# Kernel tuning notes

Hardware: AMD Instinct MI355X
Metric: run time of the kernel (lower is better)

## Reference

```python
import jax, jax.numpy as jnp
import numpy as np

MAX_SEQ = 512
HIDDEN = 1024
E = 2 * HIDDEN  # expansion
S = 128         # head dim s
EPS = 1e-5


def setup_inputs() -> dict:
    key = jax.random.key(0)
    ks = jax.random.split(key, 10)
    B, N = 32, 512
    x = jax.random.normal(ks[0], (B, N, HIDDEN), dtype=jnp.float32)
    attention_mask = jnp.ones((B, N), dtype=jnp.float32)
    gamma = jax.random.uniform(ks[1], (2, S), dtype=jnp.float32)
    beta = jax.random.uniform(ks[2], (2, S), dtype=jnp.float32)
    w = jax.random.uniform(ks[3], (2 * MAX_SEQ - 1,), dtype=jnp.float32)
    a_p = jax.random.uniform(ks[4], (1, S), dtype=jnp.float32)
    b_p = jax.random.uniform(ks[5], (1, S), dtype=jnp.float32)
    # uv: Linear(hidden -> 2e+s), stored input-major for x @ uv_w
    uv_w = jax.random.normal(ks[6], (HIDDEN, 2 * E + S), dtype=jnp.float32) * 0.02
    uv_b = jnp.zeros((2 * E + S,), dtype=jnp.float32)
    o_w = jax.random.normal(ks[7], (E, HIDDEN), dtype=jnp.float32) * 0.02
    o_b = jnp.zeros((HIDDEN,), dtype=jnp.float32)
    ln_g = jnp.ones((HIDDEN,), dtype=jnp.float32)
    ln_b = jnp.zeros((HIDDEN,), dtype=jnp.float32)
    return {"x": x, "attention_mask": attention_mask, "gamma": gamma, "beta": beta,
            "w": w, "a_p": a_p, "b_p": b_p, "uv_w": uv_w, "uv_b": uv_b,
            "o_w": o_w, "o_b": o_b, "ln_g": ln_g, "ln_b": ln_b}


def _rope_seq(x):
    # x: [b, n, 2, s]; rotary positions along axis 1 (matches module's rope(x, dim=1))
    n, d = x.shape[1], x.shape[-1]
    half = d // 2
    pos = jnp.arange(n, dtype=jnp.float32)
    # inv_freq = 10000 ** (arange(half)/half)  (freq_seq = -arange/half, inv = 10000**-freq_seq)
    inv_freq = jnp.power(10000.0, jnp.arange(half, dtype=jnp.float32) / half)
    sinusoid = pos[:, None] * inv_freq  # [n, half]
    sin = jnp.sin(sinusoid)[None, :, None, :]
    cos = jnp.cos(sinusoid)[None, :, None, :]
    x1, x2 = jnp.split(x, 2, axis=-1)
    return jnp.concatenate([x1 * cos - x2 * sin, x2 * cos + x1 * sin], axis=-1)


def _rel_pos_bias(w, seq_len):
    # Toeplitz trick (max_seq_length <= 512 path)
    t = jnp.pad(w[: 2 * MAX_SEQ - 1], (0, MAX_SEQ))          # [3S-1]
    t = jnp.tile(t, MAX_SEQ)[: -MAX_SEQ].reshape(-1, MAX_SEQ, 3 * MAX_SEQ - 2)
    r = (2 * MAX_SEQ - 1) // 2
    t = t[..., r:-r]                                          # [1, S, S]
    return t[:, :seq_len, :seq_len]


def reference(x, attention_mask, gamma, beta, w, a_p, b_p, uv_w, uv_b, o_w, o_b, ln_g, ln_b):
    n = x.shape[1]
    shortcut = x
    mu = jnp.mean(x, axis=-1, keepdims=True)
    var = jnp.mean(jnp.square(x - mu), axis=-1, keepdims=True)
    xn = (x - mu) * jax.lax.rsqrt(var + EPS) * ln_g + ln_b
    uv = jax.nn.silu(xn @ uv_w + uv_b)                        # [b, n, 2e+s]
    u, v, base = jnp.split(uv, [E, 2 * E], axis=-1)
    base = base[..., None, :] * gamma + beta                  # [b, n, 2, s]
    base = _rope_seq(base)
    q, k = base[:, :, 0], base[:, :, 1]                       # [b, n, s]
    qk = jnp.einsum('bnd,bmd->bnm', q, k)
    qk = qk + ((1.0 - attention_mask) * -1e12)[:, None, :]
    bias = _rel_pos_bias(w, n)                                # [1, n, n]
    kernel = jnp.square(jax.nn.relu(qk / MAX_SEQ + bias))
    out = u * jnp.einsum('bnm,bme->bne', kernel, v)           # [b, n, e]
    return out @ o_w + o_b + shortcut
```

## Files before the change

### kernel.cpp

```cpp
#include <hip/hip_runtime.h>
#include <math.h>

#define HIDDEN 1024
#define NSEQ   512
#define BATCH  32
#define EDIM   2048
#define SDIM   128
#define UVN    (2 * EDIM + SDIM)

using short8  = __attribute__((ext_vector_type(8))) short;
using float4x = __attribute__((ext_vector_type(4))) float;

__device__ __forceinline__ ushort f2bf(float f) {
    unsigned u = __float_as_uint(f);
    u += 0x7FFFu + ((u >> 16) & 1u);
    return (ushort)(u >> 16);
}
__device__ __forceinline__ float bf2f(ushort h) {
    return __uint_as_float(((unsigned)h) << 16);
}

#define ASYNC16(gp, lp) __builtin_amdgcn_global_load_lds( \
    (const __attribute__((address_space(1))) unsigned int*)(unsigned long long)(const void*)(gp), \
    (__attribute__((address_space(3))) unsigned int*)(unsigned int)(unsigned long long)(const void*)(lp), \
    16, 0, 0)

__global__ __launch_bounds__(64) void tab_kernel(float* __restrict__ sin_t,
                                                 float* __restrict__ cos_t) {
    int i = blockIdx.x;
    int j = threadIdx.x;
    double inv = pow(10000.0, (double)j / 64.0);
    double ang = (double)i * inv;
    sin_t[i * 64 + j] = (float)sin(ang);
    cos_t[i * 64 + j] = (float)cos(ang);
}

__global__ __launch_bounds__(256) void transpose_f32_bf16(const float* __restrict__ src,
                                                          ushort* __restrict__ dst,
                                                          int R, int Cc) {
    __shared__ float tile[32][33];
    const int bx = blockIdx.x;
    const int by = blockIdx.y;
    const int lx = threadIdx.x & 31;
    const int gy = threadIdx.x >> 5;
#pragma unroll
    for (int i = 0; i < 4; ++i) {
        int r = by * 32 + gy + i * 8;
        tile[gy + i * 8][lx] = src[(size_t)r * Cc + bx * 32 + lx];
    }
    __syncthreads();
#pragma unroll
    for (int i = 0; i < 4; ++i) {
        int c = bx * 32 + gy + i * 8;
        dst[(size_t)c * R + by * 32 + lx] = f2bf(tile[lx][gy + i * 8]);
    }
}

__global__ __launch_bounds__(256) void ln_kernel(const float* __restrict__ x,
                                                 const float* __restrict__ g,
                                                 const float* __restrict__ b,
                                                 ushort* __restrict__ xn) {
    const size_t t = blockIdx.x;
    const int tid = threadIdx.x;
    const float4 v = ((const float4*)(x + t * HIDDEN))[tid];
    float s = v.x + v.y + v.z + v.w;
#pragma unroll
    for (int off = 32; off > 0; off >>= 1) s += __shfl_down(s, off);
    __shared__ float red[4];
    const int wid = tid >> 6, lane = tid & 63;
    if (lane == 0) red[wid] = s;
    __syncthreads();
    const float mean = (red[0] + red[1] + red[2] + red[3]) * (1.0f / HIDDEN);
    __syncthreads();
    const float dx = v.x - mean, dy = v.y - mean, dz = v.z - mean, dw = v.w - mean;
    float s2 = dx * dx + dy * dy + dz * dz + dw * dw;
#pragma unroll
    for (int off = 32; off > 0; off >>= 1) s2 += __shfl_down(s2, off);
    if (lane == 0) red[wid] = s2;
    __syncthreads();
    const float var = (red[0] + red[1] + red[2] + red[3]) * (1.0f / HIDDEN);
    const float rs = rsqrtf(var + 1e-5f);
    const float4 gv = ((const float4*)g)[tid];
    const float4 bv = ((const float4*)b)[tid];
    ushort4 o;
    o.x = f2bf(dx * rs * gv.x + bv.x);
    o.y = f2bf(dy * rs * gv.y + bv.y);
    o.z = f2bf(dz * rs * gv.z + bv.z);
    o.w = f2bf(dw * rs * gv.w + bv.w);
    ((ushort4*)(xn + t * HIDDEN))[tid] = o;
}

__device__ __forceinline__ void mfma_core_128(const ushort* __restrict__ A,
                                              const ushort* __restrict__ Bt,
                                              const int lda, const int ldb, const int K,
                                              const int m0, const int n0,
                                              ushort* As, ushort* Bs,
                                              float4x (&acc)[4][4]) {
    const int tid = threadIdx.x;
    const int l = tid & 63, w = tid >> 6;
    const int wm = (w & 1) << 6, wn = (w >> 1) << 6;

    const int c0 = w * 128 + l;
    const int r0 = c0 >> 2, kc0 = (c0 & 3) * 8;
    const int c1 = c0 + 64;
    const int r1 = c1 >> 2, kc1 = (c1 & 3) * 8;
    char* ldsA0 = (char*)As + (size_t)(w * 128) * 16;
    char* ldsA1 = ldsA0 + 1024;
    char* ldsB0 = (char*)Bs + (size_t)(w * 128) * 16;
    char* ldsB1 = ldsB0 + 1024;
    const ushort* gA0 = A + (size_t)(m0 + r0) * lda + kc0;
    const ushort* gA1 = A + (size_t)(m0 + r1) * lda + kc1;
    const ushort* gB0 = Bt + (size_t)(n0 + r0) * ldb + kc0;
    const ushort* gB1 = Bt + (size_t)(n0 + r1) * ldb + kc1;

    const int lr = l & 15, lk = (l >> 4) * 8;
    int aoff[4], boff[4];
#pragma unroll
    for (int i = 0; i < 4; ++i) {
        aoff[i] = (wm + i * 16 + lr) * 32 + lk;
        boff[i] = (wn + i * 16 + lr) * 32 + lk;
    }

    for (int k0 = 0; k0 < K; k0 += 32) {
        __syncthreads();
        ASYNC16(gA0 + k0, ldsA0);
        ASYNC16(gA1 + k0, ldsA1);
        ASYNC16(gB0 + k0, ldsB0);
        ASYNC16(gB1 + k0, ldsB1);
        __syncthreads();
        short8 af[4], bfr[4];
#pragma unroll
        for (int i = 0; i < 4; ++i) af[i] = *(const short8*)(As + aoff[i]);
#pragma unroll
        for (int i = 0; i < 4; ++i) bfr[i] = *(const short8*)(Bs + boff[i]);
#pragma unroll
        for (int mi = 0; mi < 4; ++mi)
#pragma unroll
            for (int ni = 0; ni < 4; ++ni)
                acc[mi][ni] = __builtin_amdgcn_mfma_f32_16x16x32_bf16(
                    af[mi], bfr[ni], acc[mi][ni], 0, 0, 0);
    }
}

template <typename F>
__device__ __forceinline__ void epilogue_loop(const float4x (&acc)[4][4],
                                              int m0, int n0, F body) {
    const int l = threadIdx.x & 63, w = threadIdx.x >> 6;
    const int wm = (w & 1) << 6, wn = (w >> 1) << 6;
    const int lrow = (l >> 4) << 2, lcol = l & 15;
#pragma unroll
    for (int mi = 0; mi < 4; ++mi)
#pragma unroll
        for (int ni = 0; ni < 4; ++ni)
#pragma unroll
            for (int r = 0; r < 4; ++r) {
                const int m = m0 + wm + mi * 16 + lrow + r;
                const int n = n0 + wn + ni * 16 + lcol;
                body(m, n, acc[mi][ni][r]);
            }
}

__device__ __forceinline__ void mfma_core_256(const ushort* __restrict__ A,
                                              const ushort* __restrict__ Bt,
                                              const int lda, const int ldb, const int K,
                                              const int m0, const int n0,
                                              char* smem,
                                              float4x (&acc)[8][4]) {
    const int tid = threadIdx.x;
    const int l = tid & 63, w = tid >> 6;
    const int wm = w >> 2, wn = w & 3;

    const int srow = l >> 2;
    const int kcol = (w & 1) * 32 + (((tid & 3) ^ ((l >> 3) & 3)) << 3);
    const int rb0  = w >> 1;
    const ushort* gA[4];
    const ushort* gB[4];
#pragma unroll
    for (int j = 0; j < 4; ++j) {
        const int row = (j * 4 + rb0) * 16 + srow;
        gA[j] = A  + (size_t)(m0 + row) * lda + kcol;
        gB[j] = Bt + (size_t)(n0 + row) * ldb + kcol;
    }
    char* const ldsA = smem;
    char* const ldsB = smem + 65536;
    const int wdst = w * 1024;

#define STG_A(buf, j, t)  ASYNC16(gA[j] + (size_t)(t) * 64, ldsA + (buf) * 32768 + (j) * 8192 + wdst)
#define STG_B(buf, j, t)  ASYNC16(gB[j] + (size_t)(t) * 64, ldsB + (buf) * 32768 + (j) * 8192 + wdst)
#define RAWBAR() do { __builtin_amdgcn_sched_barrier(0); __builtin_amdgcn_s_barrier(); \
                      __builtin_amdgcn_sched_barrier(0); } while (0)
#define WAITV(N) asm volatile("s_waitcnt vmcnt(" #N ")" ::: "memory")

    const int LB = (l & 15) * 64 + (((l >> 4) ^ ((l >> 1) & 3)) << 4);
    const int rbbA0 = wm * 4;
    const int rbbA1 = 8 + wm * 4;
    const int cbbB0 = wn * 2;
    const int cbbB1 = 8 + wn * 2;

    const int KT = K >> 6;

    STG_A(0, 0, 0); STG_A(0, 1, 0);
    STG_B(0, 0, 0); STG_B(0, 1, 0);
    STG_B(0, 2, 0); STG_B(0, 3, 0);
    STG_A(0, 2, 0); STG_A(0, 3, 0);
    STG_A(1, 0, 1); STG_A(1, 1, 1);
    STG_B(1, 0, 1); STG_B(1, 1, 1);
    STG_B(1, 2, 1); STG_B(1, 3, 1);
    WAITV(10);
    RAWBAR();

    for (int t = 0; t < KT; ++t) {
        const int buf = t & 1;
        const char* Ab = ldsA + buf * 32768;
        const char* Bb = ldsB + buf * 32768;
        short8 a[4][2], b0[2][2], b1[2][2];

#pragma unroll
        for (int mi = 0; mi < 4; ++mi) {
            a[mi][0] = *(const short8*)(Ab + (rbbA0 + mi) * 2048 + LB);
            a[mi][1] = *(const short8*)(Ab + (rbbA0 + mi) * 2048 + 1024 + LB);
        }
#pragma unroll
        for (int ni = 0; ni < 2; ++ni) {
            b0[ni][0] = *(const short8*)(Bb + (cbbB0 + ni) * 2048 + LB);
            b0[ni][1] = *(const short8*)(Bb + (cbbB0 + ni) * 2048 + 1024 + LB);
        }
        if (t + 1 < KT) { STG_A(buf ^ 1, 2, t + 1); STG_A(buf ^ 1, 3, t + 1); }
        RAWBAR();
        __builtin_amdgcn_s_setprio(1);
#pragma unroll
        for (int mi = 0; mi < 4; ++mi)
#pragma unroll
            for (int ni = 0; ni < 2; ++ni) {
                acc[mi][ni] = __builtin_amdgcn_mfma_f32_16x16x32_bf16(a[mi][0], b0[ni][0], acc[mi][ni], 0, 0, 0);
                acc[mi][ni] = __builtin_amdgcn_mfma_f32_16x16x32_bf16(a[mi][1], b0[ni][1], acc[mi][ni], 0, 0, 0);
            }
        __builtin_amdgcn_s_setprio(0);
        if (t < KT - 1) { WAITV(10); } else { WAITV(2); }
        RAWBAR();

#pragma unroll
        for (int ni = 0; ni < 2; ++ni) {
            b1[ni][0] = *(const short8*)(Bb + (cbbB1 + ni) * 2048 + LB);
            b1[ni][1] = *(const short8*)(Bb + (cbbB1 + ni) * 2048 + 1024 + LB);
        }
        if (t + 2 < KT) { STG_A(buf, 0, t + 2); STG_A(buf, 1, t + 2); }
        RAWBAR();
        __builtin_amdgcn_s_setprio(1);
#pragma unroll
        for (int mi = 0; mi < 4; ++mi)
#pragma unroll
            for (int ni = 0; ni < 2; ++ni) {
                acc[mi][2 + ni] = __builtin_amdgcn_mfma_f32_16x16x32_bf16(a[mi][0], b1[ni][0], acc[mi][2 + ni], 0, 0, 0);
                acc[mi][2 + ni] = __builtin_amdgcn_mfma_f32_16x16x32_bf16(a[mi][1], b1[ni][1], acc[mi][2 + ni], 0, 0, 0);
            }
        __builtin_amdgcn_s_setprio(0);
        if (t < KT - 2) { WAITV(10); } else if (t == KT - 2) { WAITV(8); } else { WAITV(0); }
        RAWBAR();

#pragma unroll
        for (int mi = 0; mi < 4; ++mi) {
            a[mi][0] = *(const short8*)(Ab + (rbbA1 + mi) * 2048 + LB);
            a[mi][1] = *(const short8*)(Ab + (rbbA1 + mi) * 2048 + 1024 + LB);
        }
        if (t + 2 < KT) {
            STG_B(buf, 0, t + 2); STG_B(buf, 1, t + 2);
            STG_B(buf, 2, t + 2); STG_B(buf, 3, t + 2);
        }
        RAWBAR();
        __builtin_amdgcn_s_setprio(1);
#pragma unroll
        for (int mi = 0; mi < 4; ++mi)
#pragma unroll
            for (int ni = 0; ni < 2; ++ni) {
                acc[4 + mi][2 + ni] = __builtin_amdgcn_mfma_f32_16x16x32_bf16(a[mi][0], b1[ni][0], acc[4 + mi][2 + ni], 0, 0, 0);
                acc[4 + mi][2 + ni] = __builtin_amdgcn_mfma_f32_16x16x32_bf16(a[mi][1], b1[ni][1], acc[4 + mi][2 + ni], 0, 0, 0);
            }
#pragma unroll
        for (int mi = 0; mi < 4; ++mi)
#pragma unroll
            for (int ni = 0; ni < 2; ++ni) {
                acc[4 + mi][ni] = __builtin_amdgcn_mfma_f32_16x16x32_bf16(a[mi][0], b0[ni][0], acc[4 + mi][ni], 0, 0, 0);
                acc[4 + mi][ni] = __builtin_amdgcn_mfma_f32_16x16x32_bf16(a[mi][1], b0[ni][1], acc[4 + mi][ni], 0, 0, 0);
            }
        __builtin_amdgcn_s_setprio(0);
        if (t < KT - 2) { WAITV(10); } else if (t == KT - 2) { WAITV(4); }
        RAWBAR();
    }
#undef STG_A
#undef STG_B
#undef RAWBAR
#undef WAITV
}

template <typename F>
__device__ __forceinline__ void epilogue_256(const float4x (&acc)[8][4],
                                             int m0, int n0, F body) {
    const int tid = threadIdx.x;
    const int l = tid & 63, w = tid >> 6;
    const int wm = w >> 2, wn = w & 3;
    const int lrow = (l >> 4) << 2, lcol = l & 15;
#pragma unroll
    for (int i = 0; i < 8; ++i)
#pragma unroll
        for (int j = 0; j < 4; ++j)
#pragma unroll
            for (int r = 0; r < 4; ++r) {
                const int m = m0 + (i >> 2) * 128 + wm * 64 + (i & 3) * 16 + lrow + r;
                const int n = n0 + (j >> 1) * 128 + wn * 32 + (j & 1) * 16 + lcol;
                body(m, n, acc[i][j][r]);
            }
}

__device__ __forceinline__ void mfma_core_v3(const ushort* __restrict__ A,
                                             const ushort* __restrict__ Bt,
                                             const int lda, const int ldb, const int K,
                                             const int m0, const int n0,
                                             char* smem,
                                             float4x (&acc)[4][4]) {
    const int tid = threadIdx.x;
    const int l = tid & 63, w = tid >> 6;
    const int wm = w >> 2, wn = w & 3;

    const int srow = l >> 2;
    const int kswz = ((l & 3) ^ ((l >> 3) & 3)) << 3;
    const ushort* gA = A + (size_t)(m0 + w * 16 + srow) * lda + kswz;
    const ushort* gB = Bt + (size_t)(n0 + w * 16 + srow) * ldb + kswz;
    char* const ldsA = smem;
    char* const ldsB = smem + 65536;
    const int woff = w * 2048;

    const int LB = (l & 15) * 64 + (((l >> 4) ^ ((l >> 1) & 3)) << 4);
    const int rbb = wm * 4, cbb = wn * 4;
    const int KT = K >> 6;

    ASYNC16(gA, ldsA + woff);
    ASYNC16(gA + 32, ldsA + woff + 1024);
    ASYNC16(gB, ldsB + woff);
    ASYNC16(gB + 32, ldsB + woff + 1024);
    __syncthreads();

    for (int t = 0; t < KT; ++t) {
        const int buf = t & 1;
        const char* Ab = ldsA + buf * 32768;
        const char* Bb = ldsB + buf * 32768;
        if (t + 1 < KT) {
            const size_t g = (size_t)(t + 1) * 64;
            char* dA = ldsA + (buf ^ 1) * 32768 + woff;
            char* dB = ldsB + (buf ^ 1) * 32768 + woff;
            ASYNC16(gA + g, dA);
            ASYNC16(gA + g + 32, dA + 1024);
            ASYNC16(gB + g, dB);
            ASYNC16(gB + g + 32, dB + 1024);
        }
        __builtin_amdgcn_sched_barrier(0);
#pragma unroll
        for (int kh = 0; kh < 2; ++kh) {
            short8 a[4], b[4];
#pragma unroll
            for (int i = 0; i < 4; ++i) {
                a[i] = *(const short8*)(Ab + (rbb + i) * 2048 + kh * 1024 + LB);
                b[i] = *(const short8*)(Bb + (cbb + i) * 2048 + kh * 1024 + LB);
            }
            __builtin_amdgcn_s_setprio(1);
#pragma unroll
            for (int i = 0; i < 4; ++i)
#pragma unroll
                for (int j = 0; j < 4; ++j)
                    acc[i][j] = __builtin_amdgcn_mfma_f32_16x16x32_bf16(
                        a[i], b[j], acc[i][j], 0, 0, 0);
            __builtin_amdgcn_s_setprio(0);
        }
        __syncthreads();
    }
}

template <typename F>
__device__ __forceinline__ void epilogue_v3(const float4x (&acc)[4][4],
                                            int m0, int n0, F body) {
    const int tid = threadIdx.x;
    const int l = tid & 63, w = tid >> 6;
    const int wm = w >> 2, wn = w & 3;
    const int lrow = (l >> 4) << 2, lcol = l & 15;
#pragma unroll
    for (int i = 0; i < 4; ++i)
#pragma unroll
        for (int j = 0; j < 4; ++j)
#pragma unroll
            for (int r = 0; r < 4; ++r) {
                const int m = m0 + wm * 64 + i * 16 + lrow + r;
                const int n = n0 + wn * 64 + j * 16 + lcol;
                body(m, n, acc[i][j][r]);
            }
}

__global__ __launch_bounds__(1024, 4) void gemm_uv3(const ushort* __restrict__ A,
                                                    const ushort* __restrict__ Bt,
                                                    const float* __restrict__ bias,
                                                    ushort* __restrict__ U,
                                                    ushort* __restrict__ VT) {
    __shared__ __align__(16) char smem[131072];
    float4x acc[4][4] = {};
    const int n0 = blockIdx.x * 256, m0 = blockIdx.y * 256;
    mfma_core_v3(A, Bt, HIDDEN, HIDDEN, HIDDEN, m0, n0, smem, acc);
    if (blockIdx.x < 8) {
        epilogue_v3(acc, m0, n0, [&](int m, int n, float aval) {
            float val = aval + bias[n];
            val = val / (1.0f + expf(-val));
            U[(size_t)m * EDIM + n] = f2bf(val);
        });
    } else {
        epilogue_v3(acc, m0, n0, [&](int m, int n, float aval) {
            float val = aval + bias[n];
            val = val / (1.0f + expf(-val));
            const int e = n - EDIM;
            const int b = m >> 9;
            const int s = m & (NSEQ - 1);
            VT[((size_t)b * EDIM + e) * NSEQ + s] = f2bf(val);
        });
    }
}

__global__ __launch_bounds__(256) void gemm_base_mfma(const ushort* __restrict__ A,
                                                      const ushort* __restrict__ Bt,
                                                      const float* __restrict__ bias,
                                                      float* __restrict__ BASE) {
    __shared__ ushort As[128 * 32], Bs[128 * 32];
    float4x acc[4][4] = {};
    const int n0 = 2 * EDIM;
    const int m0 = blockIdx.y * 128;
    mfma_core_128(A, Bt, HIDDEN, HIDDEN, HIDDEN, m0, n0, As, Bs, acc);
    epilogue_loop(acc, m0, n0, [&](int m, int n, float aval) {
        float val = aval + bias[n];
        val = val / (1.0f + expf(-val));
        BASE[(size_t)m * SDIM + (n - 2 * EDIM)] = val;
    });
}

__global__ __launch_bounds__(128) void rope_kernel(const float* __restrict__ base,
                                                   const float* __restrict__ gamma,
                                                   const float* __restrict__ beta,
                                                   const float* __restrict__ sin_t,
                                                   const float* __restrict__ cos_t,
                                                   ushort* __restrict__ qh,
                                                   ushort* __restrict__ ql,
                                                   ushort* __restrict__ kh,
                                                   ushort* __restrict__ kl) {
    const size_t t = blockIdx.x;
    const int d = threadIdx.x;
    const int pos = (int)(t & (NSEQ - 1));
    __shared__ float vq[128], vk[128];
    const float bval = base[t * SDIM + d];
    vq[d] = bval * gamma[d] + beta[d];
    vk[d] = bval * gamma[SDIM + d] + beta[SDIM + d];
    __syncthreads();
    const int h = d & 63;
    const float sn = sin_t[pos * 64 + h];
    const float cs = cos_t[pos * 64 + h];
    float oq, ok;
    if (d < 64) {
        oq = vq[d] * cs - vq[d + 64] * sn;
        ok = vk[d] * cs - vk[d + 64] * sn;
    } else {
        oq = vq[d] * cs + vq[d - 64] * sn;
        ok = vk[d] * cs + vk[d - 64] * sn;
    }
    const ushort qhv = f2bf(oq);
    const ushort khv = f2bf(ok);
    qh[t * SDIM + d] = qhv;
    ql[t * SDIM + d] = f2bf(oq - bf2f(qhv));
    kh[t * SDIM + d] = khv;
    kl[t * SDIM + d] = f2bf(ok - bf2f(khv));
}

__global__ __launch_bounds__(256, 4) void gemm_qk3(const ushort* __restrict__ qh,
                                                   const ushort* __restrict__ ql,
                                                   const ushort* __restrict__ kh,
                                                   const ushort* __restrict__ kl,
                                                   const float* __restrict__ mask,
                                                   const float* __restrict__ w,
                                                   ushort* __restrict__ km) {
    __shared__ __align__(16) char smem[32768];
    float4x acc[4][4] = {};
    const int b = blockIdx.z;
    const int tid = threadIdx.x;
    const int l = tid & 63, wv = tid >> 6;
    const int wm = wv & 1, wn = wv >> 1;
    const int m0 = blockIdx.y * 128, n0 = blockIdx.x * 128;
    const size_t boff = (size_t)b * NSEQ * SDIM;

    const int srow = l >> 2;
    const int kswz = ((l & 3) ^ ((l >> 3) & 3)) << 3;
    const size_t r0 = (size_t)(m0 + wv * 16 + srow) * SDIM + kswz;
    const size_t r1 = r0 + (size_t)64 * SDIM;
    const size_t c0 = (size_t)(n0 + wv * 16 + srow) * SDIM + kswz;
    const size_t c1 = c0 + (size_t)64 * SDIM;
    const ushort* gqh = qh + boff;
    const ushort* gql = ql + boff;
    const ushort* gkh = kh + boff;
    const ushort* gkl = kl + boff;

    const int LB = (l & 15) * 64 + (((l >> 4) ^ ((l >> 1) & 3)) << 4);

    for (int t = 0; t < 4; ++t) {
        const int g = t * 32;
        ASYNC16(gqh + r0 + g, smem + wv * 1024);
        ASYNC16(gqh + r1 + g, smem + (4 + wv) * 1024);
        ASYNC16(gql + r0 + g, smem + 8192 + wv * 1024);
        ASYNC16(gql + r1 + g, smem + 8192 + (4 + wv) * 1024);
        ASYNC16(gkh + c0 + g, smem + 16384 + wv * 1024);
        ASYNC16(gkh + c1 + g, smem + 16384 + (4 + wv) * 1024);
        ASYNC16(gkl + c0 + g, smem + 24576 + wv * 1024);
        ASYNC16(gkl + c1 + g, smem + 24576 + (4 + wv) * 1024);
        __syncthreads();
        short8 ah[4], bh[4], bl[4];
#pragma unroll
        for (int i = 0; i < 4; ++i) {
            ah[i] = *(const short8*)(smem + (wm * 4 + i) * 1024 + LB);
            bh[i] = *(const short8*)(smem + 16384 + (wn * 4 + i) * 1024 + LB);
            bl[i] = *(const short8*)(smem + 24576 + (wn * 4 + i) * 1024 + LB);
        }
        __builtin_amdgcn_s_setprio(1);
#pragma unroll
        for (int i = 0; i < 4; ++i)
#pragma unroll
            for (int j = 0; j < 4; ++j) {
                acc[i][j] = __builtin_amdgcn_mfma_f32_16x16x32_bf16(ah[i], bh[j], acc[i][j], 0, 0, 0);
                acc[i][j] = __builtin_amdgcn_mfma_f32_16x16x32_bf16(ah[i], bl[j], acc[i][j], 0, 0, 0);
            }
        __builtin_amdgcn_s_setprio(0);
        short8 al[4];
#pragma unroll
        for (int i = 0; i < 4; ++i)
            al[i] = *(const short8*)(smem + 8192 + (wm * 4 + i) * 1024 + LB);
        __builtin_amdgcn_s_setprio(1);
#pragma unroll
        for (int i = 0; i < 4; ++i)
#pragma unroll
            for (int j = 0; j < 4; ++j)
                acc[i][j] = __builtin_amdgcn_mfma_f32_16x16x32_bf16(al[i], bh[j], acc[i][j], 0, 0, 0);
        __builtin_amdgcn_s_setprio(0);
        if (t < 3) __syncthreads();
    }

    const int lrow = (l >> 4) << 2, lcol = l & 15;
    const float inv512 = 1.0f / 512.0f;
#pragma unroll
    for (int i = 0; i < 4; ++i)
#pragma unroll
        for (int j = 0; j < 4; ++j)
#pragma unroll
            for (int r = 0; r < 4; ++r) {
                const int m = m0 + wm * 64 + i * 16 + lrow + r;
                const int n = n0 + wn * 64 + j * 16 + lcol;
                const float mterm = (1.0f - mask[b * NSEQ + n]) * -1e12f;
                float val = (acc[i][j][r] + mterm) * inv512 + w[511 + n - m];
                val = fmaxf(val, 0.0f);
                km[(size_t)b * NSEQ * NSEQ + (size_t)m * NSEQ + n] = f2bf(val * val);
            }
}

__global__ __launch_bounds__(512) void gemm_pv2(const ushort* __restrict__ km,
                                                const ushort* __restrict__ vT,
                                                ushort* __restrict__ ug) {
    __shared__ __align__(16) char smem[131072];
    float4x acc[8][4] = {};
    const int b = blockIdx.z;
    const int n0 = blockIdx.x * 256, m0 = blockIdx.y * 256;
    mfma_core_256(km + (size_t)b * NSEQ * NSEQ, vT + (size_t)b * EDIM * NSEQ,
                  NSEQ, NSEQ, NSEQ, m0, n0, smem, acc);
    const size_t tokbase = (size_t)b * NSEQ;
    epilogue_256(acc, m0, n0, [&](int m, int n, float aval) {
        const size_t idx = (tokbase + m) * EDIM + n;
        ug[idx] = f2bf(bf2f(ug[idx]) * aval);
    });
}

__global__ __launch_bounds__(512) void gemm_out2(const ushort* __restrict__ A,
                                                 const ushort* __restrict__ Bt,
                                                 const float* __restrict__ ob,
                                                 const float* __restrict__ x,
                                                 float* __restrict__ out) {
    __shared__ __align__(16) char smem[131072];
    float4x acc[8][4] = {};
    const int n0 = blockIdx.x * 256, m0 = blockIdx.y * 256;
    mfma_core_256(A, Bt, EDIM, EDIM, EDIM, m0, n0, smem, acc);
    epilogue_256(acc, m0, n0, [&](int m, int n, float aval) {
        out[(size_t)m * HIDDEN + n] = aval + ob[n] + x[(size_t)m * HIDDEN + n];
    });
}

extern "C" void kernel_launch(void* const* d_in, const int* in_sizes, int n_in,
                              void* d_out, int out_size, void* d_ws, size_t ws_size,
                              hipStream_t stream) {
    const float* x     = (const float*)d_in[0];
    const float* mask  = (const float*)d_in[1];
    const float* gamma = (const float*)d_in[2];
    const float* beta  = (const float*)d_in[3];
    const float* w     = (const float*)d_in[4];
    const float* uv_w  = (const float*)d_in[7];
    const float* uv_b  = (const float*)d_in[8];
    const float* o_w   = (const float*)d_in[9];
    const float* o_b   = (const float*)d_in[10];
    const float* ln_g  = (const float*)d_in[11];
    const float* ln_b  = (const float*)d_in[12];
    float* out = (float*)d_out;

    int C = 32;
    while (C > 1) {
        unsigned long long need = (unsigned long long)C * 5505024ull + 13107200ull;
        if (need <= (unsigned long long)ws_size) break;
        C >>= 1;
    }
    const int R = C * NSEQ;

    char* p = (char*)d_ws;
    ushort* xn  = (ushort*)p;  p += (size_t)C * 1048576;
    ushort* u   = (ushort*)p;  p += (size_t)C * 2097152;
    ushort* vT  = (ushort*)p;  p += (size_t)C * 2097152;
    float* base = (float*)p;   p += (size_t)C * 262144;
    float* sint = (float*)p;   p += 131072;
    float* cost = (float*)p;   p += 131072;
    ushort* uv_wt = (ushort*)p; p += 8650752;
    ushort* o_wt  = (ushort*)p; p += 4194304;
    ushort* qh = (ushort*)xn;
    ushort* ql = (ushort*)((char*)xn + (size_t)C * 131072);
    ushort* kh = (ushort*)((char*)xn + (size_t)C * 262144);
    ushort* kl = (ushort*)((char*)xn + (size_t)C * 393216);
    ushort* km = (ushort*)((char*)xn + (size_t)C * 524288);

    hipLaunchKernelGGL(tab_kernel, dim3(512), dim3(64), 0, stream, sint, cost);
    hipLaunchKernelGGL(transpose_f32_bf16, dim3(132, 32), dim3(256), 0, stream,
                       uv_w, uv_wt, HIDDEN, UVN);
    hipLaunchKernelGGL(transpose_f32_bf16, dim3(32, 64), dim3(256), 0, stream,
                       o_w, o_wt, EDIM, HIDDEN);

    for (int b0 = 0; b0 < BATCH; b0 += C) {
        const float* xc = x + (size_t)b0 * NSEQ * HIDDEN;
        float*       oc = out + (size_t)b0 * NSEQ * HIDDEN;
        const float* mc = mask + (size_t)b0 * NSEQ;
        hipLaunchKernelGGL(ln_kernel, dim3(R), dim3(256), 0, stream, xc, ln_g, ln_b, xn);
        hipLaunchKernelGGL(gemm_uv3, dim3(16, R / 256), dim3(1024), 0, stream,
                           xn, uv_wt, uv_b, u, vT);
        hipLaunchKernelGGL(gemm_base_mfma, dim3(1, R / 128), dim3(256), 0, stream,
                           xn, uv_wt, uv_b, base);
        hipLaunchKernelGGL(rope_kernel, dim3(R), dim3(128), 0, stream,
                           base, gamma, beta, sint, cost, qh, ql, kh, kl);
        hipLaunchKernelGGL(gemm_qk3, dim3(4, 4, C), dim3(256), 0, stream,
                           qh, ql, kh, kl, mc, w, km);
        hipLaunchKernelGGL(gemm_pv2, dim3(8, 2, C), dim3(512), 0, stream, km, vT, u);
        hipLaunchKernelGGL(gemm_out2, dim3(4, R / 256), dim3(512), 0, stream,
                           u, o_wt, o_b, xc, oc);
    }
}
```

Measured before the change: 518.2 us.

## Merge prep kernels, fold base GEMM into uv GEMM, switch out-proj core

The two weight transposes and the sin/cos table are merged into one prep kernel launch. The separate base-projection GEMM is folded into gemm_uv3 as a 17th column tile that bounds-checks n < UVN, because the 256-wide tile runs past the 128 real base columns. The output projection moves from the 512-thread mfma_core_256 path to the 1024-thread mfma_core_v3 core with smaller per-thread accumulators. These changes cut launch overhead and aim to improve occupancy, at the cost of wasted MFMA work in the padded base tile.

```diff
diff --git a/kernel.cpp b/kernel.cpp
--- a/kernel.cpp
+++ b/kernel.cpp
@@ -25,22 +25,10 @@
     (__attribute__((address_space(3))) unsigned int*)(unsigned int)(unsigned long long)(const void*)(lp), \
     16, 0, 0)
 
-__global__ __launch_bounds__(64) void tab_kernel(float* __restrict__ sin_t,
-                                                 float* __restrict__ cos_t) {
-    int i = blockIdx.x;
-    int j = threadIdx.x;
-    double inv = pow(10000.0, (double)j / 64.0);
-    double ang = (double)i * inv;
-    sin_t[i * 64 + j] = (float)sin(ang);
-    cos_t[i * 64 + j] = (float)cos(ang);
-}
-
-__global__ __launch_bounds__(256) void transpose_f32_bf16(const float* __restrict__ src,
-                                                          ushort* __restrict__ dst,
-                                                          int R, int Cc) {
-    __shared__ float tile[32][33];
-    const int bx = blockIdx.x;
-    const int by = blockIdx.y;
+__device__ __forceinline__ void transpose_tile(const float* __restrict__ src,
+                                               ushort* __restrict__ dst,
+                                               int R, int Cc, int bx, int by,
+                                               float (*tile)[33]) {
     const int lx = threadIdx.x & 31;
     const int gy = threadIdx.x >> 5;
 #pragma unroll
@@ -53,6 +41,30 @@
     for (int i = 0; i < 4; ++i) {
         int c = bx * 32 + gy + i * 8;
         dst[(size_t)c * R + by * 32 + lx] = f2bf(tile[lx][gy + i * 8]);
+    }
+}
+
+__global__ __launch_bounds__(256) void prep_kernel(const float* __restrict__ uv_w,
+                                                   ushort* __restrict__ uv_wt,
+                                                   const float* __restrict__ o_w,
+                                                   ushort* __restrict__ o_wt,
+                                                   float* __restrict__ sin_t,
+                                                   float* __restrict__ cos_t) {
+    __shared__ float tile[32][33];
+    const int blk = blockIdx.x;
+    if (blk < 4224) {
+        transpose_tile(uv_w, uv_wt, HIDDEN, UVN, blk % 132, blk / 132, tile);
+    } else if (blk < 6272) {
+        const int r = blk - 4224;
+        transpose_tile(o_w, o_wt, EDIM, HIDDEN, r % 32, r / 32, tile);
+    } else {
+        const int r = blk - 6272;
+        const int i = r * 4 + (threadIdx.x >> 6);
+        const int j = threadIdx.x & 63;
+        double inv = pow(10000.0, (double)j / 64.0);
+        double ang = (double)i * inv;
+        sin_t[i * 64 + j] = (float)sin(ang);
+        cos_t[i * 64 + j] = (float)cos(ang);
     }
 }
 
@@ -90,76 +102,6 @@
     ((ushort4*)(xn + t * HIDDEN))[tid] = o;
 }
 
-__device__ __forceinline__ void mfma_core_128(const ushort* __restrict__ A,
-                                              const ushort* __restrict__ Bt,
-                                              const int lda, const int ldb, const int K,
-                                              const int m0, const int n0,
-                                              ushort* As, ushort* Bs,
-                                              float4x (&acc)[4][4]) {
-    const int tid = threadIdx.x;
-    const int l = tid & 63, w = tid >> 6;
-    const int wm = (w & 1) << 6, wn = (w >> 1) << 6;
-
-    const int c0 = w * 128 + l;
-    const int r0 = c0 >> 2, kc0 = (c0 & 3) * 8;
-    const int c1 = c0 + 64;
-    const int r1 = c1 >> 2, kc1 = (c1 & 3) * 8;
-    char* ldsA0 = (char*)As + (size_t)(w * 128) * 16;
-    char* ldsA1 = ldsA0 + 1024;
-    char* ldsB0 = (char*)Bs + (size_t)(w * 128) * 16;
-    char* ldsB1 = ldsB0 + 1024;
-    const ushort* gA0 = A + (size_t)(m0 + r0) * lda + kc0;
-    const ushort* gA1 = A + (size_t)(m0 + r1) * lda + kc1;
-    const ushort* gB0 = Bt + (size_t)(n0 + r0) * ldb + kc0;
-    const ushort* gB1 = Bt + (size_t)(n0 + r1) * ldb + kc1;
-
-    const int lr = l & 15, lk = (l >> 4) * 8;
-    int aoff[4], boff[4];
-#pragma unroll
-    for (int i = 0; i < 4; ++i) {
-        aoff[i] = (wm + i * 16 + lr) * 32 + lk;
-        boff[i] = (wn + i * 16 + lr) * 32 + lk;
-    }
-
-    for (int k0 = 0; k0 < K; k0 += 32) {
-        __syncthreads();
-        ASYNC16(gA0 + k0, ldsA0);
-        ASYNC16(gA1 + k0, ldsA1);
-        ASYNC16(gB0 + k0, ldsB0);
-        ASYNC16(gB1 + k0, ldsB1);
-        __syncthreads();
-        short8 af[4], bfr[4];
-#pragma unroll
-        for (int i = 0; i < 4; ++i) af[i] = *(const short8*)(As + aoff[i]);
-#pragma unroll
-        for (int i = 0; i < 4; ++i) bfr[i] = *(const short8*)(Bs + boff[i]);
-#pragma unroll
-        for (int mi = 0; mi < 4; ++mi)
-#pragma unroll
-            for (int ni = 0; ni < 4; ++ni)
-                acc[mi][ni] = __builtin_amdgcn_mfma_f32_16x16x32_bf16(
-                    af[mi], bfr[ni], acc[mi][ni], 0, 0, 0);
-    }
-}
-
-template <typename F>
-__device__ __forceinline__ void epilogue_loop(const float4x (&acc)[4][4],
-                                              int m0, int n0, F body) {
-    const int l = threadIdx.x & 63, w = threadIdx.x >> 6;
-    const int wm = (w & 1) << 6, wn = (w >> 1) << 6;
-    const int lrow = (l >> 4) << 2, lcol = l & 15;
-#pragma unroll
-    for (int mi = 0; mi < 4; ++mi)
-#pragma unroll
-        for (int ni = 0; ni < 4; ++ni)
-#pragma unroll
-            for (int r = 0; r < 4; ++r) {
-                const int m = m0 + wm + mi * 16 + lrow + r;
-                const int n = n0 + wn + ni * 16 + lcol;
-                body(m, n, acc[mi][ni][r]);
-            }
-}
-
 __device__ __forceinline__ void mfma_core_256(const ushort* __restrict__ A,
                                               const ushort* __restrict__ Bt,
                                               const int lda, const int ldb, const int K,
@@ -398,7 +340,8 @@
                                                     const ushort* __restrict__ Bt,
                                                     const float* __restrict__ bias,
                                                     ushort* __restrict__ U,
-                                                    ushort* __restrict__ VT) {
+                                                    ushort* __restrict__ VT,
+                                                    float* __restrict__ BASE) {
     __shared__ __align__(16) char smem[131072];
     float4x acc[4][4] = {};
     const int n0 = blockIdx.x * 256, m0 = blockIdx.y * 256;
@@ -409,7 +352,7 @@
             val = val / (1.0f + expf(-val));
             U[(size_t)m * EDIM + n] = f2bf(val);
         });
-    } else {
+    } else if (blockIdx.x < 16) {
         epilogue_v3(acc, m0, n0, [&](int m, int n, float aval) {
             float val = aval + bias[n];
             val = val / (1.0f + expf(-val));
@@ -418,23 +361,15 @@
             const int s = m & (NSEQ - 1);
             VT[((size_t)b * EDIM + e) * NSEQ + s] = f2bf(val);
         });
-    }
-}
-
-__global__ __launch_bounds__(256) void gemm_base_mfma(const ushort* __restrict__ A,
-                                                      const ushort* __restrict__ Bt,
-                                                      const float* __restrict__ bias,
-                                                      float* __restrict__ BASE) {
-    __shared__ ushort As[128 * 32], Bs[128 * 32];
-    float4x acc[4][4] = {};
-    const int n0 = 2 * EDIM;
-    const int m0 = blockIdx.y * 128;
-    mfma_core_128(A, Bt, HIDDEN, HIDDEN, HIDDEN, m0, n0, As, Bs, acc);
-    epilogue_loop(acc, m0, n0, [&](int m, int n, float aval) {
-        float val = aval + bias[n];
-        val = val / (1.0f + expf(-val));
-        BASE[(size_t)m * SDIM + (n - 2 * EDIM)] = val;
-    });
+    } else {
+        epilogue_v3(acc, m0, n0, [&](int m, int n, float aval) {
+            if (n < UVN) {
+                float val = aval + bias[n];
+                val = val / (1.0f + expf(-val));
+                BASE[(size_t)m * SDIM + (n - 2 * EDIM)] = val;
+            }
+        });
+    }
 }
 
 __global__ __launch_bounds__(128) void rope_kernel(const float* __restrict__ base,
@@ -576,16 +511,16 @@
     });
 }
 
-__global__ __launch_bounds__(512) void gemm_out2(const ushort* __restrict__ A,
-                                                 const ushort* __restrict__ Bt,
-                                                 const float* __restrict__ ob,
-                                                 const float* __restrict__ x,
-                                                 float* __restrict__ out) {
+__global__ __launch_bounds__(1024, 4) void gemm_out5(const ushort* __restrict__ A,
+                                                     const ushort* __restrict__ Bt,
+                                                     const float* __restrict__ ob,
+                                                     const float* __restrict__ x,
+                                                     float* __restrict__ out) {
     __shared__ __align__(16) char smem[131072];
-    float4x acc[8][4] = {};
+    float4x acc[4][4] = {};
     const int n0 = blockIdx.x * 256, m0 = blockIdx.y * 256;
-    mfma_core_256(A, Bt, EDIM, EDIM, EDIM, m0, n0, smem, acc);
-    epilogue_256(acc, m0, n0, [&](int m, int n, float aval) {
+    mfma_core_v3(A, Bt, EDIM, EDIM, EDIM, m0, n0, smem, acc);
+    epilogue_v3(acc, m0, n0, [&](int m, int n, float aval) {
         out[(size_t)m * HIDDEN + n] = aval + ob[n] + x[(size_t)m * HIDDEN + n];
     });
 }
@@ -629,27 +564,22 @@
     ushort* kl = (ushort*)((char*)xn + (size_t)C * 393216);
     ushort* km = (ushort*)((char*)xn + (size_t)C * 524288);
 
-    hipLaunchKernelGGL(tab_kernel, dim3(512), dim3(64), 0, stream, sint, cost);
-    hipLaunchKernelGGL(transpose_f32_bf16, dim3(132, 32), dim3(256), 0, stream,
-                       uv_w, uv_wt, HIDDEN, UVN);
-    hipLaunchKernelGGL(transpose_f32_bf16, dim3(32, 64), dim3(256), 0, stream,
-                       o_w, o_wt, EDIM, HIDDEN);
+    hipLaunchKernelGGL(prep_kernel, dim3(6400), dim3(256), 0, stream,
+                       uv_w, uv_wt, o_w, o_wt, sint, cost);
 
     for (int b0 = 0; b0 < BATCH; b0 += C) {
         const float* xc = x + (size_t)b0 * NSEQ * HIDDEN;
         float*       oc = out + (size_t)b0 * NSEQ * HIDDEN;
         const float* mc = mask + (size_t)b0 * NSEQ;
         hipLaunchKernelGGL(ln_kernel, dim3(R), dim3(256), 0, stream, xc, ln_g, ln_b, xn);
-        hipLaunchKernelGGL(gemm_uv3, dim3(16, R / 256), dim3(1024), 0, stream,
-                           xn, uv_wt, uv_b, u, vT);
-        hipLaunchKernelGGL(gemm_base_mfma, dim3(1, R / 128), dim3(256), 0, stream,
-                           xn, uv_wt, uv_b, base);
+        hipLaunchKernelGGL(gemm_uv3, dim3(17, R / 256), dim3(1024), 0, stream,
+                           xn, uv_wt, uv_b, u, vT, base);
         hipLaunchKernelGGL(rope_kernel, dim3(R), dim3(128), 0, stream,
                            base, gamma, beta, sint, cost, qh, ql, kh, kl);
         hipLaunchKernelGGL(gemm_qk3, dim3(4, 4, C), dim3(256), 0, stream,
                            qh, ql, kh, kl, mc, w, km);
         hipLaunchKernelGGL(gemm_pv2, dim3(8, 2, C), dim3(512), 0, stream, km, vT, u);
-        hipLaunchKernelGGL(gemm_out2, dim3(4, R / 256), dim3(512), 0, stream,
+        hipLaunchKernelGGL(gemm_out5, dim3(4, R / 256), dim3(1024), 0, stream,
                            u, o_wt, o_b, xc, oc);
     }
 }
```

New measurement: 559.8 us. 8.0% more time.
